# Optimization experiments

Measured on AMD Instinct MI355X. Metric: run time of the kernel, lower is better.

The kernel has to match this reference:

```python
import jax, jax.numpy as jnp
import numpy as np

H = 1024  # hidden_size == input_size
L = 2     # num_layers


def _gru_cell(x, h, W_ih, W_hh, b_ih, b_hh):
    # PyTorch GRUCell math. x:[B,D], h:[B,H]
    gi = x @ W_ih.T + b_ih          # [B,3H]
    gh = h @ W_hh.T + b_hh          # [B,3H]
    i_r, i_z, i_n = jnp.split(gi, 3, axis=-1)
    h_r, h_z, h_n = jnp.split(gh, 3, axis=-1)
    r = jax.nn.sigmoid(i_r + h_r)
    z = jax.nn.sigmoid(i_z + h_z)
    n = jnp.tanh(i_n + r * h_n)
    return (1.0 - z) * n + z * h


def setup_inputs() -> dict:
    key = jax.random.key(0)
    ks = jax.random.split(key, 16)
    B, T = 64, 256
    s = 0.05
    x = jax.random.normal(ks[0], (B, T, H), dtype=jnp.float32)
    h0 = jnp.zeros((1, H), dtype=jnp.float32)
    lengths = jnp.maximum(jax.random.randint(ks[1], (B,), 0, T + 1), 1).astype(jnp.int32)
    W_ih = jax.random.normal(ks[2], (L, 3 * H, H), dtype=jnp.float32) * s
    W_hh = jax.random.normal(ks[3], (L, 3 * H, H), dtype=jnp.float32) * s
    b_ih = jax.random.normal(ks[4], (L, 3 * H), dtype=jnp.float32) * s
    b_hh = jax.random.normal(ks[5], (L, 3 * H), dtype=jnp.float32) * s
    gW1 = jax.random.normal(ks[6], (H, H), dtype=jnp.float32) * s
    gb1 = jax.random.normal(ks[7], (H,), dtype=jnp.float32) * s
    gW2 = jax.random.normal(ks[8], (H, H), dtype=jnp.float32) * s
    gb2 = jax.random.normal(ks[9], (H,), dtype=jnp.float32) * s
    gWF = jax.random.normal(ks[10], (1, H), dtype=jnp.float32) * s
    gbF = jax.random.normal(ks[11], (1,), dtype=jnp.float32) * s
    return {"x": x, "h0": h0, "input_lengths": lengths,
            "W_ih": W_ih, "W_hh": W_hh, "b_ih": b_ih, "b_hh": b_hh,
            "gW1": gW1, "gb1": gb1, "gW2": gW2, "gb2": gb2,
            "gWF": gWF, "gbF": gbF}


def reference(x, h0, input_lengths, W_ih, W_hh, b_ih, b_hh, gW1, gb1, gW2, gb2, gWF, gbF):
    B, T, _ = x.shape
    h0b = jnp.broadcast_to(h0, (B, H))                      # [B,H]
    init_h = jnp.broadcast_to(h0b[None], (L, B, H))         # [L,B,H]
    x_t = jnp.swapaxes(x, 0, 1)                             # [T,B,D]
    x_next = jnp.concatenate([x_t[1:], x_t[-1:]], axis=0)   # x[t+1], last repeated (unused)
    ts = jnp.arange(T, dtype=jnp.int32)

    def step(ht, inp):
        xt, xnext, t = inp
        cur = xt
        new_h = []
        for n in range(L):  # dropout is identity at inference
            hn = _gru_cell(cur, ht[n], W_ih[n], W_hh[n], b_ih[n], b_hh[n])
            new_h.append(hn)
            cur = hn
        ht_new = jnp.stack(new_h)                           # [L,B,H]
        out_t = cur                                         # [B,H]
        # BinaryGate(x_{t+1}, ht_n)
        y = xnext @ gW1.T + gb1 + out_t @ gW2.T + gb2       # [B,H]
        g_raw = jax.nn.sigmoid(y @ gWF.T + gbF)[:, 0]       # [B]
        is_last = t == (input_lengths - 1)
        gt = jnp.where(is_last, 1.0, g_raw)
        valid = t < input_lengths
        out_m = jnp.where(valid[:, None], out_t, 0.0)
        gt_m = jnp.where(valid, gt, 0.0)
        reset = (gt > 0.5) & valid
        ht_next = jnp.where(reset[None, :, None], h0b[None], ht_new)
        ht_next = jnp.where(valid[None, :, None], ht_next, ht)
        return ht_next, (out_m, gt_m)

    _, (outs, gates) = jax.lax.scan(step, init_h, (x_t, x_next, ts))
    output = jnp.swapaxes(outs, 0, 1)                       # [B,T,H]
    gate_z = jnp.swapaxes(gates, 0, 1)                      # [B,T]
    return output, gate_z
```

## Files before the change

### kernel.cpp

```cpp
#include <hip/hip_runtime.h>
#include <cmath>

#define Bsz 64
#define Tsz 256
#define Hsz 1024
#define NWG 256
#define NTHR 512
#define GRPWG 64
#define WROW 522

#define WAITVM(N) do {                                            \
    asm volatile("s_waitcnt vmcnt(" #N ")" ::: "memory");         \
    __builtin_amdgcn_sched_barrier(0);                            \
} while (0)

__device__ float g_h[2][2][Bsz * Hsz];
__device__ float g_pre[2][Bsz];
__device__ float g_an[Tsz * Bsz];
__device__ float g_v1[Hsz];
__device__ float g_v2[Hsz];
__device__ float g_c;
__device__ unsigned g_bar_cnt[4 * 32];
__device__ unsigned g_bar_gen[4 * 32];
__device__ float g_gi0[(size_t)Tsz * Bsz * 3 * Hsz];

__device__ __forceinline__ float ldc(const float* p) {
    return __hip_atomic_load((const float*)p, __ATOMIC_RELAXED,
                             __HIP_MEMORY_SCOPE_AGENT);
}
__device__ __forceinline__ void stc(float* p, float v) {
    __hip_atomic_store(p, v, __ATOMIC_RELAXED, __HIP_MEMORY_SCOPE_AGENT);
}

__device__ __forceinline__ void ldc4_issue(const float* p, float4& v) {
    asm volatile("global_load_dwordx4 %0, %1, off sc0 sc1"
                 : "=v"(v) : "v"(p));
}

__device__ __forceinline__ float4 bfx4(uint2 u) {
    float4 f;
    f.x = __uint_as_float(u.x << 16);
    f.y = __uint_as_float(u.x & 0xffff0000u);
    f.z = __uint_as_float(u.y << 16);
    f.w = __uint_as_float(u.y & 0xffff0000u);
    return f;
}

__device__ __forceinline__ unsigned rne_bf16_pair(float a, float b) {
    unsigned u0 = __float_as_uint(a);
    unsigned u1 = __float_as_uint(b);
    u0 = (u0 + 0x7fffu + ((u0 >> 16) & 1u)) >> 16;
    u1 = (u1 + 0x7fffu + ((u1 >> 16) & 1u)) >> 16;
    return u0 | (u1 << 16);
}

__device__ __forceinline__ void groupbar(int bg, unsigned lgen) {
    __syncthreads();
    if (threadIdx.x == 0) {
        unsigned* cnt = &g_bar_cnt[bg * 32];
        unsigned* gen = &g_bar_gen[bg * 32];
        unsigned prev = __hip_atomic_fetch_add(cnt, 1u, __ATOMIC_RELAXED,
                                               __HIP_MEMORY_SCOPE_AGENT);
        if (prev == lgen * GRPWG - 1u) {
            __hip_atomic_store(gen, lgen, __ATOMIC_RELAXED,
                               __HIP_MEMORY_SCOPE_AGENT);
        } else {
            while (__hip_atomic_load(gen, __ATOMIC_RELAXED,
                                     __HIP_MEMORY_SCOPE_AGENT) < lgen)
                __builtin_amdgcn_s_sleep(1);
        }
    }
    __syncthreads();
}

__global__ void k_init(const float* __restrict__ h0,
                       const float* __restrict__ gW1, const float* __restrict__ gb1,
                       const float* __restrict__ gW2, const float* __restrict__ gb2,
                       const float* __restrict__ gWF, const float* __restrict__ gbF) {
    int blk = blockIdx.x, tid = threadIdx.x;
    if (blk < 256) {
        int idx = blk * 256 + tid;
        float v = h0[idx & (Hsz - 1)];
        g_h[0][0][idx] = v;
        g_h[1][0][idx] = v;
    } else if (blk == 256) {
        __shared__ float red[256];
        float s = 0.f;
        for (int j = tid; j < Hsz; j += 256) s += gWF[j] * (gb1[j] + gb2[j]);
        red[tid] = s;
        __syncthreads();
        for (int off = 128; off > 0; off >>= 1) {
            if (tid < off) red[tid] += red[tid + off];
            __syncthreads();
        }
        if (tid == 0) g_c = red[0] + gbF[0];
        if (tid < 128) ((float*)g_pre)[tid] = 0.f;
        if (tid >= 128 && tid < 256) {
            g_bar_cnt[tid - 128] = 0u;
            g_bar_gen[tid - 128] = 0u;
        }
    } else if (blk < 261) {
        int k = (blk - 257) * 256 + tid;
        float s = 0.f;
        for (int j = 0; j < Hsz; ++j) s += gWF[j] * gW1[(size_t)j * Hsz + k];
        g_v1[k] = s;
    } else {
        int k = (blk - 261) * 256 + tid;
        float s = 0.f;
        for (int j = 0; j < Hsz; ++j) s += gWF[j] * gW2[(size_t)j * Hsz + k];
        g_v2[k] = s;
    }
}

__global__ void k_an(const float* __restrict__ x) {
    int blk = blockIdx.x, tid = threadIdx.x;
    int lane = tid & 63, wv = tid >> 6;
    for (int i = 0; i < 16; ++i) {
        int o = blk * 64 + wv * 16 + i;
        int b = o >> 8, tt = o & 255;
        int ts = (tt + 1 < Tsz) ? tt + 1 : Tsz - 1;
        const float* xp = x + ((size_t)b * Tsz + ts) * Hsz;
        float s = 0.f;
        for (int k = lane; k < Hsz; k += 64) s += xp[k] * g_v1[k];
        for (int m = 32; m > 0; m >>= 1) s += __shfl_xor(s, m, 64);
        if (lane == 0) g_an[tt * 64 + b] = s;
    }
}

__global__ __launch_bounds__(256) void k_gemm(const float* __restrict__ x,
                                              const float* __restrict__ Wih,
                                              const float* __restrict__ bih) {
    __shared__ float As[16][132];
    __shared__ float Bs[16][132];
    const int tid = threadIdx.x;
    const int n0 = blockIdx.x * 128;
    const int m0 = blockIdx.y * 128;
    const int tx = tid & 15, ty = tid >> 4;
    float acc[8][8] = {};

    for (int k0 = 0; k0 < Hsz; k0 += 16) {
#pragma unroll
        for (int i = 0; i < 2; ++i) {
            int task = tid * 2 + i;
            int rl = task >> 2;
            int kq = task & 3;
            int r = m0 + rl;
            int bb = r & 63, tt = r >> 6;
            float4 v = *(const float4*)(x + ((size_t)bb * Tsz + tt) * Hsz + k0 + kq * 4);
            As[kq * 4 + 0][rl] = v.x; As[kq * 4 + 1][rl] = v.y;
            As[kq * 4 + 2][rl] = v.z; As[kq * 4 + 3][rl] = v.w;
            float4 w = *(const float4*)(Wih + (size_t)(n0 + rl) * Hsz + k0 + kq * 4);
            Bs[kq * 4 + 0][rl] = w.x; Bs[kq * 4 + 1][rl] = w.y;
            Bs[kq * 4 + 2][rl] = w.z; Bs[kq * 4 + 3][rl] = w.w;
        }
        __syncthreads();
#pragma unroll
        for (int k = 0; k < 16; ++k) {
            float a[8], b[8];
            *(float4*)&a[0] = *(float4*)&As[k][ty * 8];
            *(float4*)&a[4] = *(float4*)&As[k][ty * 8 + 4];
            *(float4*)&b[0] = *(float4*)&Bs[k][tx * 8];
            *(float4*)&b[4] = *(float4*)&Bs[k][tx * 8 + 4];
#pragma unroll
            for (int i2 = 0; i2 < 8; ++i2)
#pragma unroll
                for (int j2 = 0; j2 < 8; ++j2) acc[i2][j2] += a[i2] * b[j2];
        }
        __syncthreads();
    }
#pragma unroll
    for (int i2 = 0; i2 < 8; ++i2) {
        int r = m0 + ty * 8 + i2;
        float* cp = g_gi0 + (size_t)r * (3 * Hsz) + n0 + tx * 8;
#pragma unroll
        for (int j2 = 0; j2 < 8; j2 += 4) {
            float4 v;
            v.x = acc[i2][j2 + 0] + bih[n0 + tx * 8 + j2 + 0];
            v.y = acc[i2][j2 + 1] + bih[n0 + tx * 8 + j2 + 1];
            v.z = acc[i2][j2 + 2] + bih[n0 + tx * 8 + j2 + 2];
            v.w = acc[i2][j2 + 3] + bih[n0 + tx * 8 + j2 + 3];
            *(float4*)(cp + j2) = v;
        }
    }
}

__device__ __forceinline__ float dot4(float4 a, float4 b) {
    return a.x * b.x + a.y * b.y + a.z * b.z + a.w * b.w;
}

template <bool IS_L1>
__device__ __forceinline__ void do_phase(
    int t, int b0, int jn0,
    const float* __restrict__ a0,
    const float* __restrict__ st, float* __restrict__ ho,
    const float* __restrict__ Wi, const float* __restrict__ Wh,
    const float* __restrict__ bi, const float* __restrict__ bh,
    const float* __restrict__ h0, const int* __restrict__ lens,
    float* __restrict__ outp, const unsigned* s_wl,
    float (*s_act)[2][16][36], float (*s_red)[4][16][16],
    const float* __restrict__ s_rst, float (*s_gs)[16]) {

    const int tid = threadIdx.x;
    const int wv = tid >> 6, lane = tid & 63;
    const int bi2 = (lane & 7) * 2, ji2 = (lane >> 3) * 2;
    const int kq0 = wv * 128;

    const float* wph[6];
    const float* wpi[6];
    int rb[6];
#pragma unroll
    for (int g = 0; g < 3; ++g)
#pragma unroll
        for (int dj = 0; dj < 2; ++dj) {
            if constexpr (IS_L1) {
                int row = g * Hsz + jn0 + ji2 + dj;
                wph[g * 2 + dj] = Wh + (size_t)row * Hsz;
                wpi[g * 2 + dj] = Wi + (size_t)row * Hsz;
            } else {
                rb[g * 2 + dj] = (g * 16 + ji2 + dj) * WROW;
            }
        }

    constexpr int NR = IS_L1 ? 4 : 2;
    constexpr int NM = IS_L1 ? 4 : 3;
    float acc[NM][2][2] = {};

    auto issue_chunk = [&](int c, float4* dst) {
        const int kb = kq0 + c * 32;
#pragma unroll
        for (int i = 0; i < NR; ++i) {
            int o = i * 64 + lane;
            int ts = o >> 7;
            int bb = (o >> 3) & 15, k4 = o & 7;
            int k = kb + k4 * 4;
            const float* p = (IS_L1 && ts == 0)
                ? (a0 + (size_t)(b0 + bb) * Hsz + k)
                : (st + (size_t)(b0 + bb) * Hsz + k);
            ldc4_issue(p, dst[i]);
        }
    };
    auto patch_write = [&](int c, float4* src) {
        const int kb = kq0 + c * 32;
#pragma unroll
        for (int i = 0; i < NR; ++i) {
            int o = i * 64 + lane;
            int ts = IS_L1 ? (o >> 7) : 0;
            int bb = (o >> 3) & 15, k4 = o & 7;
            int k = kb + k4 * 4;
            float4 v = src[i];
            if (!(IS_L1 && ts == 0)) {
                float4 hv = *(const float4*)(h0 + k);
                if (s_rst[bb] != 0.f) v = hv;
            }
            *(float4*)&s_act[wv][ts][bb][k4 * 4] = v;
        }
    };
    auto compute_chunk = [&](int c) {
        const int kb = kq0 + c * 32;
#pragma unroll 2
        for (int kk = 0; kk < 32; kk += 4) {
            const int k = kb + kk;
            const int hs = IS_L1 ? 1 : 0;
            float4 hA = *(const float4*)&s_act[wv][hs][bi2][kk];
            float4 hB = *(const float4*)&s_act[wv][hs][bi2 + 1][kk];
            if constexpr (IS_L1) {
                float4 xA = *(const float4*)&s_act[wv][0][bi2][kk];
                float4 xB = *(const float4*)&s_act[wv][0][bi2 + 1][kk];
#pragma unroll
                for (int dj = 0; dj < 2; ++dj) {
                    float4 whr = *(const float4*)(wph[0 * 2 + dj] + k);
                    float4 whz = *(const float4*)(wph[1 * 2 + dj] + k);
                    float4 whn = *(const float4*)(wph[2 * 2 + dj] + k);
                    float4 wir = *(const float4*)(wpi[0 * 2 + dj] + k);
                    float4 wiz = *(const float4*)(wpi[1 * 2 + dj] + k);
                    float4 win = *(const float4*)(wpi[2 * 2 + dj] + k);
                    acc[0][0][dj] += dot4(xA, wir) + dot4(hA, whr);
                    acc[0][1][dj] += dot4(xB, wir) + dot4(hB, whr);
                    acc[1][0][dj] += dot4(xA, wiz) + dot4(hA, whz);
                    acc[1][1][dj] += dot4(xB, wiz) + dot4(hB, whz);
                    acc[2][0][dj] += dot4(xA, win);
                    acc[2][1][dj] += dot4(xB, win);
                    acc[3][0][dj] += dot4(hA, whn);
                    acc[3][1][dj] += dot4(hB, whn);
                }
            } else {
                const int kw = k >> 1;
#pragma unroll
                for (int dj = 0; dj < 2; ++dj) {
                    float4 whr = bfx4(*(const uint2*)&s_wl[rb[0 * 2 + dj] + kw]);
                    float4 whz = bfx4(*(const uint2*)&s_wl[rb[1 * 2 + dj] + kw]);
                    float4 whn = bfx4(*(const uint2*)&s_wl[rb[2 * 2 + dj] + kw]);
                    acc[0][0][dj] += dot4(hA, whr);
                    acc[0][1][dj] += dot4(hB, whr);
                    acc[1][0][dj] += dot4(hA, whz);
                    acc[1][1][dj] += dot4(hB, whz);
                    acc[2][0][dj] += dot4(hA, whn);
                    acc[2][1][dj] += dot4(hB, whn);
                }
            }
        }
    };

    float4 C0[NR], C1[NR], C2[NR], C3[NR];
    issue_chunk(0, C0);
    issue_chunk(1, C1);
    issue_chunk(2, C2);
    issue_chunk(3, C3);
    if constexpr (IS_L1) WAITVM(12); else WAITVM(6);
    patch_write(0, C0); compute_chunk(0);
    if constexpr (IS_L1) WAITVM(8);  else WAITVM(4);
    patch_write(1, C1); compute_chunk(1);
    if constexpr (IS_L1) WAITVM(4);  else WAITVM(2);
    patch_write(2, C2); compute_chunk(2);
    WAITVM(0);
    patch_write(3, C3); compute_chunk(3);

    __syncthreads();
    if (wv >= 4) {
#pragma unroll
        for (int m = 0; m < NM; ++m)
#pragma unroll
            for (int db = 0; db < 2; ++db)
#pragma unroll
                for (int dj = 0; dj < 2; ++dj)
                    s_red[wv - 4][m][bi2 + db][ji2 + dj] = acc[m][db][dj];
    }
    __syncthreads();
    if (wv < 4) {
#pragma unroll
        for (int m = 0; m < NM; ++m)
#pragma unroll
            for (int db = 0; db < 2; ++db)
#pragma unroll
                for (int dj = 0; dj < 2; ++dj)
                    s_red[wv][m][bi2 + db][ji2 + dj] += acc[m][db][dj];
    }
    __syncthreads();

    if (tid < 256) {
        const int ji = tid & 15, bI = tid >> 4;
        const int b = b0 + bI, jn = jn0 + ji;
        float hprev = ldc(st + (size_t)b * Hsz + jn);
        const int lb = lens[b];
        float s[NM];
#pragma unroll
        for (int m = 0; m < NM; ++m)
            s[m] = s_red[0][m][bI][ji] + s_red[1][m][bI][ji] +
                   s_red[2][m][bI][ji] + s_red[3][m][bI][ji];
        if (s_rst[bI] != 0.f) hprev = h0[jn];

        float pr, pz, pin, phn;
        if constexpr (IS_L1) {
            pr  = s[0] + bi[jn] + bh[jn];
            pz  = s[1] + bi[Hsz + jn] + bh[Hsz + jn];
            pin = s[2] + bi[2 * Hsz + jn];
            phn = s[3] + bh[2 * Hsz + jn];
        } else {
            const float* gp = g_gi0 + (size_t)(t * 64 + b) * (3 * Hsz) + jn;
            float g0r = gp[0];
            float g0z = gp[Hsz];
            float g0n = gp[2 * Hsz];
            pr  = g0r + s[0] + bh[jn];
            pz  = g0z + s[1] + bh[Hsz + jn];
            pin = g0n;
            phn = s[2] + bh[2 * Hsz + jn];
        }
        const float r_ = 1.f / (1.f + __expf(-pr));
        const float z_ = 1.f / (1.f + __expf(-pz));
        const float n_ = tanhf(pin + r_ * phn);
        const float hnew = (1.f - z_) * n_ + z_ * hprev;
        stc(ho + (size_t)b * Hsz + jn, hnew);
        if constexpr (IS_L1) {
            outp[((size_t)b * Tsz + t) * Hsz + jn] = (t < lb) ? hnew : 0.f;
            s_gs[bI][ji] = hnew * g_v2[jn];
        }
    }
    if constexpr (IS_L1) {
        __syncthreads();
        if (tid < 16) {
            float sm = 0.f;
#pragma unroll
            for (int j = 0; j < 16; ++j) sm += s_gs[tid][j];
            atomicAdd(&g_pre[t & 1][b0 + tid], sm);
        }
    }
}

__global__ void __launch_bounds__(NTHR, 1)
k_main(const float* __restrict__ h0, const int* __restrict__ lens,
       const float* __restrict__ W_ih, const float* __restrict__ W_hh,
       const float* __restrict__ b_ih, const float* __restrict__ b_hh,
       float* __restrict__ outp, float* __restrict__ gatep) {
    __shared__ __align__(16) unsigned s_w[48 * WROW];
    __shared__ __align__(16) float s_act[8][2][16][36];
    __shared__ float s_red[4][4][16][16];
    __shared__ float s_rst[16];
    __shared__ float s_gs[16][16];

    const int tid = threadIdx.x;
    const int wg = blockIdx.x, bg = wg >> 6, jg = wg & 63;
    const int b0 = bg * 16, jn0 = jg * 16;
    unsigned lgen = 0;

    const float* Wih1 = W_ih + (size_t)3 * Hsz * Hsz;
    const float* Whh1 = W_hh + (size_t)3 * Hsz * Hsz;
    const float* bi1 = b_ih + 3 * Hsz;
    const float* bh1 = b_hh + 3 * Hsz;

    for (int idx = tid; idx < 48 * 512; idx += NTHR) {
        int r = idx >> 9, kw = idx & 511;
        int g = r >> 4, j = r & 15;
        const float* wrow = W_hh + ((size_t)(g * Hsz + jn0 + j)) * Hsz + kw * 2;
        s_w[r * WROW + kw] = rne_bf16_pair(wrow[0], wrow[1]);
    }
    __syncthreads();

    for (int t = 0; t < Tsz; ++t) {
        const int p0 = t & 1, p1 = p0 ^ 1;

        if (tid < 16) {
            float rstf = 0.f;
            const int b = b0 + tid;
            const int lb = lens[b];
            if (t > 0) {
                const int tp = t - 1;
                const float pre = g_c + g_an[tp * 64 + b] + ldc(&g_pre[p1][b]);
                const bool il = (tp == lb - 1);
                rstf = (il || pre > 0.f) ? 1.f : 0.f;
                if (jg == 0) {
                    const float gt = il ? 1.f : 1.f / (1.f + __expf(-pre));
                    gatep[(size_t)b * Tsz + tp] = (tp < lb) ? gt : 0.f;
                }
            }
            s_rst[tid] = rstf;
        }
        __syncthreads();

        do_phase<false>(t, b0, jn0, nullptr,
                        g_h[0][p0], g_h[0][p1],
                        W_ih, W_hh, b_ih, b_hh, h0, lens,
                        outp, s_w, s_act, s_red, s_rst, s_gs);
        groupbar(bg, ++lgen);

        if (jg == 0 && tid < 16) stc(&g_pre[p1][b0 + tid], 0.f);

        do_phase<true>(t, b0, jn0, g_h[0][p1],
                       g_h[1][p0], g_h[1][p1],
                       Wih1, Whh1, bi1, bh1, h0, lens,
                       outp, s_w, s_act, s_red, s_rst, s_gs);
        groupbar(bg, ++lgen);
    }

    if (jg == 0 && tid < 16) {
        const int b = b0 + tid;
        const int lb = lens[b];
        const int tp = Tsz - 1;
        const float pre = g_c + g_an[tp * 64 + b] + ldc(&g_pre[tp & 1][b]);
        const bool il = (tp == lb - 1);
        const float gt = il ? 1.f : 1.f / (1.f + __expf(-pre));
        gatep[(size_t)b * Tsz + tp] = (tp < lb) ? gt : 0.f;
    }
}

extern "C" void kernel_launch(void* const* d_in, const int* in_sizes, int n_in,
                              void* d_out, int out_size, void* d_ws, size_t ws_size,
                              hipStream_t stream) {
    const float* x = (const float*)d_in[0];
    const float* h0 = (const float*)d_in[1];
    const int* lens = (const int*)d_in[2];
    const float* W_ih = (const float*)d_in[3];
    const float* W_hh = (const float*)d_in[4];
    const float* b_ih = (const float*)d_in[5];
    const float* b_hh = (const float*)d_in[6];
    const float* gW1 = (const float*)d_in[7];
    const float* gb1 = (const float*)d_in[8];
    const float* gW2 = (const float*)d_in[9];
    const float* gb2 = (const float*)d_in[10];
    const float* gWF = (const float*)d_in[11];
    const float* gbF = (const float*)d_in[12];
    float* outp = (float*)d_out;
    float* gatep = outp + (size_t)Bsz * Tsz * Hsz;

    hipLaunchKernelGGL(k_init, dim3(265), dim3(256), 0, stream,
                       h0, gW1, gb1, gW2, gb2, gWF, gbF);
    hipLaunchKernelGGL(k_an, dim3(256), dim3(256), 0, stream, x);
    hipLaunchKernelGGL(k_gemm, dim3(24, 128), dim3(256), 0, stream,
                       x, W_ih, b_ih);

    void* args[8] = { (void*)&h0, (void*)&lens, (void*)&W_ih, (void*)&W_hh,
                      (void*)&b_ih, (void*)&b_hh, (void*)&outp, (void*)&gatep };
    hipError_t err = hipLaunchCooperativeKernel((const void*)k_main, dim3(NWG), dim3(NTHR),
                                                args, 0, stream);
    (void)err;
}
```

Baseline: 14.37 ms.

## Move layer-1 recurrent matvec into layer-0 phase to shorten the critical path

Layer 1's hidden-to-hidden product (W_hh1 · h1_prev) does not depend on layer 0's new output. It is now computed in phase A, alongside layer 0's recurrent matvec, and kept in registers until phase B. Phase B then only computes W_ih1 · h0_new before reducing and applying the gates. This balances the work between the two barrier-separated phases and shortens the phase that follows the layer-0 barrier, at the cost of more registers and more global weight traffic in phase A.

```diff
diff --git a/kernel.cpp b/kernel.cpp
--- a/kernel.cpp
+++ b/kernel.cpp
@@ -188,71 +188,65 @@
     return a.x * b.x + a.y * b.y + a.z * b.z + a.w * b.w;
 }
 
-template <bool IS_L1>
-__device__ __forceinline__ void do_phase(
+__device__ __forceinline__ void phaseA(
     int t, int b0, int jn0,
-    const float* __restrict__ a0,
-    const float* __restrict__ st, float* __restrict__ ho,
-    const float* __restrict__ Wi, const float* __restrict__ Wh,
-    const float* __restrict__ bi, const float* __restrict__ bh,
-    const float* __restrict__ h0, const int* __restrict__ lens,
-    float* __restrict__ outp, const unsigned* s_wl,
+    const float* __restrict__ st0, float* __restrict__ ho0,
+    const float* __restrict__ st1,
+    const float* __restrict__ Whh1,
+    const float* __restrict__ bh0,
+    const float* __restrict__ h0,
+    const unsigned* s_wl,
     float (*s_act)[2][16][36], float (*s_red)[4][16][16],
-    const float* __restrict__ s_rst, float (*s_gs)[16]) {
+    const float* __restrict__ s_rst,
+    float (&axh)[3][2][2]) {
 
     const int tid = threadIdx.x;
     const int wv = tid >> 6, lane = tid & 63;
     const int bi2 = (lane & 7) * 2, ji2 = (lane >> 3) * 2;
     const int kq0 = wv * 128;
 
-    const float* wph[6];
-    const float* wpi[6];
     int rb[6];
+    const float* wp1[6];
 #pragma unroll
     for (int g = 0; g < 3; ++g)
 #pragma unroll
         for (int dj = 0; dj < 2; ++dj) {
-            if constexpr (IS_L1) {
-                int row = g * Hsz + jn0 + ji2 + dj;
-                wph[g * 2 + dj] = Wh + (size_t)row * Hsz;
-                wpi[g * 2 + dj] = Wi + (size_t)row * Hsz;
-            } else {
-                rb[g * 2 + dj] = (g * 16 + ji2 + dj) * WROW;
-            }
-        }
-
-    constexpr int NR = IS_L1 ? 4 : 2;
-    constexpr int NM = IS_L1 ? 4 : 3;
-    float acc[NM][2][2] = {};
+            rb[g * 2 + dj] = (g * 16 + ji2 + dj) * WROW;
+            wp1[g * 2 + dj] = Whh1 + (size_t)(g * Hsz + jn0 + ji2 + dj) * Hsz;
+        }
+
+    float acc0[3][2][2] = {};
+#pragma unroll
+    for (int m = 0; m < 3; ++m)
+#pragma unroll
+        for (int a = 0; a < 2; ++a)
+#pragma unroll
+            for (int d = 0; d < 2; ++d) axh[m][a][d] = 0.f;
 
     auto issue_chunk = [&](int c, float4* dst) {
         const int kb = kq0 + c * 32;
 #pragma unroll
-        for (int i = 0; i < NR; ++i) {
-            int o = i * 64 + lane;
-            int ts = o >> 7;
+        for (int i = 0; i < 4; ++i) {
+            int o = (i & 1) * 64 + lane;
+            int layer = i >> 1;
             int bb = (o >> 3) & 15, k4 = o & 7;
             int k = kb + k4 * 4;
-            const float* p = (IS_L1 && ts == 0)
-                ? (a0 + (size_t)(b0 + bb) * Hsz + k)
-                : (st + (size_t)(b0 + bb) * Hsz + k);
+            const float* p = (layer ? st1 : st0) + (size_t)(b0 + bb) * Hsz + k;
             ldc4_issue(p, dst[i]);
         }
     };
     auto patch_write = [&](int c, float4* src) {
         const int kb = kq0 + c * 32;
 #pragma unroll
-        for (int i = 0; i < NR; ++i) {
-            int o = i * 64 + lane;
-            int ts = IS_L1 ? (o >> 7) : 0;
+        for (int i = 0; i < 4; ++i) {
+            int o = (i & 1) * 64 + lane;
+            int layer = i >> 1;
             int bb = (o >> 3) & 15, k4 = o & 7;
             int k = kb + k4 * 4;
             float4 v = src[i];
-            if (!(IS_L1 && ts == 0)) {
-                float4 hv = *(const float4*)(h0 + k);
-                if (s_rst[bb] != 0.f) v = hv;
-            }
-            *(float4*)&s_act[wv][ts][bb][k4 * 4] = v;
+            float4 hv = *(const float4*)(h0 + k);
+            if (s_rst[bb] != 0.f) v = hv;
+            *(float4*)&s_act[wv][layer][bb][k4 * 4] = v;
         }
     };
     auto compute_chunk = [&](int c) {
@@ -260,57 +254,43 @@
 #pragma unroll 2
         for (int kk = 0; kk < 32; kk += 4) {
             const int k = kb + kk;
-            const int hs = IS_L1 ? 1 : 0;
-            float4 hA = *(const float4*)&s_act[wv][hs][bi2][kk];
-            float4 hB = *(const float4*)&s_act[wv][hs][bi2 + 1][kk];
-            if constexpr (IS_L1) {
-                float4 xA = *(const float4*)&s_act[wv][0][bi2][kk];
-                float4 xB = *(const float4*)&s_act[wv][0][bi2 + 1][kk];
-#pragma unroll
-                for (int dj = 0; dj < 2; ++dj) {
-                    float4 whr = *(const float4*)(wph[0 * 2 + dj] + k);
-                    float4 whz = *(const float4*)(wph[1 * 2 + dj] + k);
-                    float4 whn = *(const float4*)(wph[2 * 2 + dj] + k);
-                    float4 wir = *(const float4*)(wpi[0 * 2 + dj] + k);
-                    float4 wiz = *(const float4*)(wpi[1 * 2 + dj] + k);
-                    float4 win = *(const float4*)(wpi[2 * 2 + dj] + k);
-                    acc[0][0][dj] += dot4(xA, wir) + dot4(hA, whr);
-                    acc[0][1][dj] += dot4(xB, wir) + dot4(hB, whr);
-                    acc[1][0][dj] += dot4(xA, wiz) + dot4(hA, whz);
-                    acc[1][1][dj] += dot4(xB, wiz) + dot4(hB, whz);
-                    acc[2][0][dj] += dot4(xA, win);
-                    acc[2][1][dj] += dot4(xB, win);
-                    acc[3][0][dj] += dot4(hA, whn);
-                    acc[3][1][dj] += dot4(hB, whn);
-                }
-            } else {
-                const int kw = k >> 1;
-#pragma unroll
-                for (int dj = 0; dj < 2; ++dj) {
-                    float4 whr = bfx4(*(const uint2*)&s_wl[rb[0 * 2 + dj] + kw]);
-                    float4 whz = bfx4(*(const uint2*)&s_wl[rb[1 * 2 + dj] + kw]);
-                    float4 whn = bfx4(*(const uint2*)&s_wl[rb[2 * 2 + dj] + kw]);
-                    acc[0][0][dj] += dot4(hA, whr);
-                    acc[0][1][dj] += dot4(hB, whr);
-                    acc[1][0][dj] += dot4(hA, whz);
-                    acc[1][1][dj] += dot4(hB, whz);
-                    acc[2][0][dj] += dot4(hA, whn);
-                    acc[2][1][dj] += dot4(hB, whn);
-                }
+            const int kw = k >> 1;
+            float4 hA = *(const float4*)&s_act[wv][0][bi2][kk];
+            float4 hB = *(const float4*)&s_act[wv][0][bi2 + 1][kk];
+            float4 gA = *(const float4*)&s_act[wv][1][bi2][kk];
+            float4 gB = *(const float4*)&s_act[wv][1][bi2 + 1][kk];
+#pragma unroll
+            for (int dj = 0; dj < 2; ++dj) {
+                float4 whr = bfx4(*(const uint2*)&s_wl[rb[0 * 2 + dj] + kw]);
+                float4 whz = bfx4(*(const uint2*)&s_wl[rb[1 * 2 + dj] + kw]);
+                float4 whn = bfx4(*(const uint2*)&s_wl[rb[2 * 2 + dj] + kw]);
+                acc0[0][0][dj] += dot4(hA, whr);
+                acc0[0][1][dj] += dot4(hB, whr);
+                acc0[1][0][dj] += dot4(hA, whz);
+                acc0[1][1][dj] += dot4(hB, whz);
+                acc0[2][0][dj] += dot4(hA, whn);
+                acc0[2][1][dj] += dot4(hB, whn);
+                float4 w1r = *(const float4*)(wp1[0 * 2 + dj] + k);
+                float4 w1z = *(const float4*)(wp1[1 * 2 + dj] + k);
+                float4 w1n = *(const float4*)(wp1[2 * 2 + dj] + k);
+                axh[0][0][dj] += dot4(gA, w1r);
+                axh[0][1][dj] += dot4(gB, w1r);
+                axh[1][0][dj] += dot4(gA, w1z);
+                axh[1][1][dj] += dot4(gB, w1z);
+                axh[2][0][dj] += dot4(gA, w1n);
+                axh[2][1][dj] += dot4(gB, w1n);
             }
         }
     };
 
-    float4 C0[NR], C1[NR], C2[NR], C3[NR];
-    issue_chunk(0, C0);
-    issue_chunk(1, C1);
-    issue_chunk(2, C2);
-    issue_chunk(3, C3);
-    if constexpr (IS_L1) WAITVM(12); else WAITVM(6);
+    float4 C0[4], C1[4], C2[4], C3[4];
+    issue_chunk(0, C0); issue_chunk(1, C1);
+    issue_chunk(2, C2); issue_chunk(3, C3);
+    WAITVM(12);
     patch_write(0, C0); compute_chunk(0);
-    if constexpr (IS_L1) WAITVM(8);  else WAITVM(4);
+    WAITVM(8);
     patch_write(1, C1); compute_chunk(1);
-    if constexpr (IS_L1) WAITVM(4);  else WAITVM(2);
+    WAITVM(4);
     patch_write(2, C2); compute_chunk(2);
     WAITVM(0);
     patch_write(3, C3); compute_chunk(3);
@@ -318,22 +298,160 @@
     __syncthreads();
     if (wv >= 4) {
 #pragma unroll
-        for (int m = 0; m < NM; ++m)
+        for (int m = 0; m < 3; ++m)
 #pragma unroll
             for (int db = 0; db < 2; ++db)
 #pragma unroll
                 for (int dj = 0; dj < 2; ++dj)
-                    s_red[wv - 4][m][bi2 + db][ji2 + dj] = acc[m][db][dj];
+                    s_red[wv - 4][m][bi2 + db][ji2 + dj] = acc0[m][db][dj];
     }
     __syncthreads();
     if (wv < 4) {
 #pragma unroll
-        for (int m = 0; m < NM; ++m)
+        for (int m = 0; m < 3; ++m)
 #pragma unroll
             for (int db = 0; db < 2; ++db)
 #pragma unroll
                 for (int dj = 0; dj < 2; ++dj)
-                    s_red[wv][m][bi2 + db][ji2 + dj] += acc[m][db][dj];
+                    s_red[wv][m][bi2 + db][ji2 + dj] += acc0[m][db][dj];
+    }
+    __syncthreads();
+
+    if (tid < 256) {
+        const int ji = tid & 15, bI = tid >> 4;
+        const int b = b0 + bI, jn = jn0 + ji;
+        float hprev = ldc(st0 + (size_t)b * Hsz + jn);
+        const float* gp = g_gi0 + (size_t)(t * 64 + b) * (3 * Hsz) + jn;
+        float g0r = gp[0];
+        float g0z = gp[Hsz];
+        float g0n = gp[2 * Hsz];
+        float s[3];
+#pragma unroll
+        for (int m = 0; m < 3; ++m)
+            s[m] = s_red[0][m][bI][ji] + s_red[1][m][bI][ji] +
+                   s_red[2][m][bI][ji] + s_red[3][m][bI][ji];
+        if (s_rst[bI] != 0.f) hprev = h0[jn];
+
+        const float pr  = g0r + s[0] + bh0[jn];
+        const float pz  = g0z + s[1] + bh0[Hsz + jn];
+        const float pin = g0n;
+        const float phn = s[2] + bh0[2 * Hsz + jn];
+        const float r_ = 1.f / (1.f + __expf(-pr));
+        const float z_ = 1.f / (1.f + __expf(-pz));
+        const float n_ = tanhf(pin + r_ * phn);
+        const float hnew = (1.f - z_) * n_ + z_ * hprev;
+        stc(ho0 + (size_t)b * Hsz + jn, hnew);
+    }
+}
+
+__device__ __forceinline__ void phaseB(
+    int t, int b0, int jn0,
+    const float* __restrict__ a0,
+    const float* __restrict__ st, float* __restrict__ ho,
+    const float* __restrict__ Wih1,
+    const float* __restrict__ bi, const float* __restrict__ bh,
+    const float* __restrict__ h0, const int* __restrict__ lens,
+    float* __restrict__ outp,
+    float (*s_act)[2][16][36], float (*s_red)[4][16][16],
+    const float* __restrict__ s_rst, float (*s_gs)[16],
+    const float (&axh)[3][2][2]) {
+
+    const int tid = threadIdx.x;
+    const int wv = tid >> 6, lane = tid & 63;
+    const int bi2 = (lane & 7) * 2, ji2 = (lane >> 3) * 2;
+    const int kq0 = wv * 128;
+
+    const float* wpi[6];
+#pragma unroll
+    for (int g = 0; g < 3; ++g)
+#pragma unroll
+        for (int dj = 0; dj < 2; ++dj)
+            wpi[g * 2 + dj] = Wih1 + (size_t)(g * Hsz + jn0 + ji2 + dj) * Hsz;
+
+    float acc[3][2][2] = {};
+
+    auto issue_chunk = [&](int c, float4* dst) {
+        const int kb = kq0 + c * 32;
+#pragma unroll
+        for (int i = 0; i < 2; ++i) {
+            int o = i * 64 + lane;
+            int bb = (o >> 3) & 15, k4 = o & 7;
+            int k = kb + k4 * 4;
+            ldc4_issue(a0 + (size_t)(b0 + bb) * Hsz + k, dst[i]);
+        }
+    };
+    auto write_chunk = [&](int c, float4* src) {
+#pragma unroll
+        for (int i = 0; i < 2; ++i) {
+            int o = i * 64 + lane;
+            int bb = (o >> 3) & 15, k4 = o & 7;
+            *(float4*)&s_act[wv][0][bb][k4 * 4] = src[i];
+        }
+    };
+    auto compute_chunk = [&](int c) {
+        const int kb = kq0 + c * 32;
+#pragma unroll 2
+        for (int kk = 0; kk < 32; kk += 4) {
+            const int k = kb + kk;
+            float4 xA = *(const float4*)&s_act[wv][0][bi2][kk];
+            float4 xB = *(const float4*)&s_act[wv][0][bi2 + 1][kk];
+#pragma unroll
+            for (int dj = 0; dj < 2; ++dj) {
+                float4 wir = *(const float4*)(wpi[0 * 2 + dj] + k);
+                float4 wiz = *(const float4*)(wpi[1 * 2 + dj] + k);
+                float4 win = *(const float4*)(wpi[2 * 2 + dj] + k);
+                acc[0][0][dj] += dot4(xA, wir);
+                acc[0][1][dj] += dot4(xB, wir);
+                acc[1][0][dj] += dot4(xA, wiz);
+                acc[1][1][dj] += dot4(xB, wiz);
+                acc[2][0][dj] += dot4(xA, win);
+                acc[2][1][dj] += dot4(xB, win);
+            }
+        }
+    };
+
+    float4 C0[2], C1[2], C2[2], C3[2];
+    issue_chunk(0, C0); issue_chunk(1, C1);
+    issue_chunk(2, C2); issue_chunk(3, C3);
+    WAITVM(6);
+    write_chunk(0, C0); compute_chunk(0);
+    WAITVM(4);
+    write_chunk(1, C1); compute_chunk(1);
+    WAITVM(2);
+    write_chunk(2, C2); compute_chunk(2);
+    WAITVM(0);
+    write_chunk(3, C3); compute_chunk(3);
+
+    float m4[4][2][2];
+#pragma unroll
+    for (int db = 0; db < 2; ++db)
+#pragma unroll
+        for (int dj = 0; dj < 2; ++dj) {
+            m4[0][db][dj] = acc[0][db][dj] + axh[0][db][dj];
+            m4[1][db][dj] = acc[1][db][dj] + axh[1][db][dj];
+            m4[2][db][dj] = acc[2][db][dj];
+            m4[3][db][dj] = axh[2][db][dj];
+        }
+
+    __syncthreads();
+    if (wv >= 4) {
+#pragma unroll
+        for (int m = 0; m < 4; ++m)
+#pragma unroll
+            for (int db = 0; db < 2; ++db)
+#pragma unroll
+                for (int dj = 0; dj < 2; ++dj)
+                    s_red[wv - 4][m][bi2 + db][ji2 + dj] = m4[m][db][dj];
+    }
+    __syncthreads();
+    if (wv < 4) {
+#pragma unroll
+        for (int m = 0; m < 4; ++m)
+#pragma unroll
+            for (int db = 0; db < 2; ++db)
+#pragma unroll
+                for (int dj = 0; dj < 2; ++dj)
+                    s_red[wv][m][bi2 + db][ji2 + dj] += m4[m][db][dj];
     }
     __syncthreads();
 
@@ -342,47 +460,31 @@
         const int b = b0 + bI, jn = jn0 + ji;
         float hprev = ldc(st + (size_t)b * Hsz + jn);
         const int lb = lens[b];
-        float s[NM];
-#pragma unroll
-        for (int m = 0; m < NM; ++m)
+        float s[4];
+#pragma unroll
+        for (int m = 0; m < 4; ++m)
             s[m] = s_red[0][m][bI][ji] + s_red[1][m][bI][ji] +
                    s_red[2][m][bI][ji] + s_red[3][m][bI][ji];
         if (s_rst[bI] != 0.f) hprev = h0[jn];
 
-        float pr, pz, pin, phn;
-        if constexpr (IS_L1) {
-            pr  = s[0] + bi[jn] + bh[jn];
-            pz  = s[1] + bi[Hsz + jn] + bh[Hsz + jn];
-            pin = s[2] + bi[2 * Hsz + jn];
-            phn = s[3] + bh[2 * Hsz + jn];
-        } else {
-            const float* gp = g_gi0 + (size_t)(t * 64 + b) * (3 * Hsz) + jn;
-            float g0r = gp[0];
-            float g0z = gp[Hsz];
-            float g0n = gp[2 * Hsz];
-            pr  = g0r + s[0] + bh[jn];
-            pz  = g0z + s[1] + bh[Hsz + jn];
-            pin = g0n;
-            phn = s[2] + bh[2 * Hsz + jn];
-        }
+        const float pr  = s[0] + bi[jn] + bh[jn];
+        const float pz  = s[1] + bi[Hsz + jn] + bh[Hsz + jn];
+        const float pin = s[2] + bi[2 * Hsz + jn];
+        const float phn = s[3] + bh[2 * Hsz + jn];
         const float r_ = 1.f / (1.f + __expf(-pr));
         const float z_ = 1.f / (1.f + __expf(-pz));
         const float n_ = tanhf(pin + r_ * phn);
         const float hnew = (1.f - z_) * n_ + z_ * hprev;
         stc(ho + (size_t)b * Hsz + jn, hnew);
-        if constexpr (IS_L1) {
-            outp[((size_t)b * Tsz + t) * Hsz + jn] = (t < lb) ? hnew : 0.f;
-            s_gs[bI][ji] = hnew * g_v2[jn];
-        }
-    }
-    if constexpr (IS_L1) {
-        __syncthreads();
-        if (tid < 16) {
-            float sm = 0.f;
-#pragma unroll
-            for (int j = 0; j < 16; ++j) sm += s_gs[tid][j];
-            atomicAdd(&g_pre[t & 1][b0 + tid], sm);
-        }
+        outp[((size_t)b * Tsz + t) * Hsz + jn] = (t < lb) ? hnew : 0.f;
+        s_gs[bI][ji] = hnew * g_v2[jn];
+    }
+    __syncthreads();
+    if (tid < 16) {
+        float sm = 0.f;
+#pragma unroll
+        for (int j = 0; j < 16; ++j) sm += s_gs[tid][j];
+        atomicAdd(&g_pre[t & 1][b0 + tid], sm);
     }
 }
 
@@ -414,6 +516,8 @@
         s_w[r * WROW + kw] = rne_bf16_pair(wrow[0], wrow[1]);
     }
     __syncthreads();
+
+    float axh[3][2][2];
 
     for (int t = 0; t < Tsz; ++t) {
         const int p0 = t & 1, p1 = p0 ^ 1;
@@ -436,18 +540,17 @@
         }
         __syncthreads();
 
-        do_phase<false>(t, b0, jn0, nullptr,
-                        g_h[0][p0], g_h[0][p1],
-                        W_ih, W_hh, b_ih, b_hh, h0, lens,
-                        outp, s_w, s_act, s_red, s_rst, s_gs);
+        phaseA(t, b0, jn0,
+               g_h[0][p0], g_h[0][p1], g_h[1][p0],
+               Whh1, b_hh, h0, s_w, s_act, s_red, s_rst, axh);
         groupbar(bg, ++lgen);
 
         if (jg == 0 && tid < 16) stc(&g_pre[p1][b0 + tid], 0.f);
 
-        do_phase<true>(t, b0, jn0, g_h[0][p1],
-                       g_h[1][p0], g_h[1][p1],
-                       Wih1, Whh1, bi1, bh1, h0, lens,
-                       outp, s_w, s_act, s_red, s_rst, s_gs);
+        phaseB(t, b0, jn0,
+               g_h[0][p1], g_h[1][p0], g_h[1][p1],
+               Wih1, bi1, bh1, h0, lens,
+               outp, s_act, s_red, s_rst, s_gs, axh);
         groupbar(bg, ++lgen);
     }
 
```

New measurement: 13.00 ms. 1.11x faster.
